# Optimization experiments

Hardware: AMD Instinct MI355X
Metric: run time of the kernel (lower is better)

Reference implementation:

```python
import jax, jax.numpy as jnp
import numpy as np

N_NODES = 10000
N_EDGES = 200000
STEPS = 2


def setup_inputs() -> dict:
    key = jax.random.key(0)
    ks = jax.random.split(key, 32)

    def w(k, shape):
        return jax.random.normal(k, shape, dtype=jnp.float32) * 0.05

    inp = {
        "x": jax.random.normal(ks[0], (N_NODES, 128), dtype=jnp.float32),
        "edge_attr": jax.random.normal(ks[1], (N_EDGES, 64), dtype=jnp.float32),
        "edge_index": jax.random.randint(ks[2], (2, N_EDGES), 0, N_NODES, dtype=jnp.int32),
        # node embedding MLP: 128 -> 128 -> 128 (ReLU after each, end_with_relu=True)
        "Wne1": w(ks[3], (128, 128)), "bne1": jnp.zeros((128,), jnp.float32),
        "Wne2": w(ks[4], (128, 128)), "bne2": jnp.zeros((128,), jnp.float32),
        # edge embedding MLP: 64 -> 128 -> 128
        "Wee1": w(ks[5], (64, 128)), "bee1": jnp.zeros((128,), jnp.float32),
        "Wee2": w(ks[6], (128, 128)), "bee2": jnp.zeros((128,), jnp.float32),
        # mlp_edge: (2*128*2 + 128*2)=768 -> 512 -> 128, ReLU after each
        "We1": w(ks[7], (768, 512)), "be1": jnp.zeros((512,), jnp.float32),
        "We2": w(ks[8], (512, 128)), "be2": jnp.zeros((128,), jnp.float32),
        # mlp_node: (128*2 + 128)=384 -> 128, ReLU
        "Wn1": w(ks[9], (384, 128)), "bn1": jnp.zeros((128,), jnp.float32),
        # update_mlp: 128 -> 128, ReLU
        "Wu": w(ks[10], (128, 128)), "bu": jnp.zeros((128,), jnp.float32),
        # node classification: 128 -> 128 (ReLU) -> 1
        "Wnc1": w(ks[11], (128, 128)), "bnc1": jnp.zeros((128,), jnp.float32),
        "Wnc2": w(ks[12], (128, 1)), "bnc2": jnp.zeros((1,), jnp.float32),
        # edge classification: 128 -> 128 (ReLU) -> 1
        "Wec1": w(ks[13], (128, 128)), "bec1": jnp.zeros((128,), jnp.float32),
        "Wec2": w(ks[14], (128, 1)), "bec2": jnp.zeros((1,), jnp.float32),
    }
    return inp


def reference(x, edge_attr, edge_index,
              Wne1, bne1, Wne2, bne2,
              Wee1, bee1, Wee2, bee2,
              We1, be1, We2, be2,
              Wn1, bn1, Wu, bu,
              Wnc1, bnc1, Wnc2, bnc2,
              Wec1, bec1, Wec2, bec2):
    relu = jax.nn.relu
    N = x.shape[0]
    j, i = edge_index[0], edge_index[1]  # j = source, i = target

    nf = relu(relu(x @ Wne1 + bne1) @ Wne2 + bne2)            # [N, 128]
    ef = relu(relu(edge_attr @ Wee1 + bee1) @ Wee2 + bee2)    # [E, 128]
    nf0, ef0 = nf, ef

    for _ in range(STEPS):
        # skip connections: concat initial features
        nfc = jnp.concatenate([nf0, nf], axis=1)   # [N, 256]
        efc = jnp.concatenate([ef0, ef], axis=1)   # [E, 256]
        x_i = nfc[i]                               # [E, 256] gather (target)
        x_j = nfc[j]                               # [E, 256] gather (source)
        # mlp_edge on [x_i, x_j, e_ij] -> new edge features [E, 128]
        e = relu(relu(jnp.concatenate([x_i, x_j, efc], axis=1) @ We1 + be1) @ We2 + be2)
        # message: mlp_node on [x_i, edge_attr] -> [E, 128]
        m = relu(jnp.concatenate([x_i, e], axis=1) @ Wn1 + bn1)
        # aggregate (add) messages at target nodes i
        agg = jax.ops.segment_sum(m, i, num_segments=N)       # [N, 128]
        # update MLP
        nf = relu(agg @ Wu + bu)
        ef = e

    preds_node = jnp.squeeze(relu(nf @ Wnc1 + bnc1) @ Wnc2 + bnc2)  # [N]
    preds_edge = jnp.squeeze(relu(ef @ Wec1 + bec1) @ Wec2 + bec2)  # [E]
    return (preds_edge, preds_node)
```

## Files before the change

kernel.cpp:

```cpp
#include <hip/hip_runtime.h>
#include <hip/hip_bf16.h>

#define N_NODES 10000
#define N_EDGES 200000
#define TE 32

typedef __attribute__((ext_vector_type(8))) short short8;
typedef __attribute__((ext_vector_type(4))) float f32x4;

static __device__ __forceinline__ ushort f2bf(float x) {
  union { float f; uint u; } v; v.f = x;
  uint r = v.u + 0x7FFF + ((v.u >> 16) & 1);
  return (ushort)(r >> 16);
}
static __device__ __forceinline__ float bf2f(ushort h) {
  union { uint u; float f; } v; v.u = ((uint)h) << 16;
  return v.f;
}

__global__ __launch_bounds__(256) void permute_w2(
    const float* __restrict__ W, ushort* __restrict__ Wp,
    int K, int N, int ld, int row0, int n0, int Ntot)
{
  int o = blockIdx.x * 256 + threadIdx.x;
  if (o >= K * N) return;
  int k = o & 31;
  int n = (o >> 5) % N;
  int kt = o / (N * 32);
  Wp[(size_t)kt * Ntot * 32 + (size_t)(n0 + n) * 32 + k] =
      f2bf(W[(size_t)(row0 + kt * 32 + k) * ld + n]);
}

template <int K1>
__global__ __launch_bounds__(256) void mlp2_kernel(
    const float* __restrict__ in, int n_rows,
    const float* __restrict__ W1, const float* __restrict__ b1,
    const float* __restrict__ W2, const float* __restrict__ b2,
    ushort* __restrict__ out0, ushort* __restrict__ out1)
{
  __shared__ float s_a[8][K1];
  __shared__ float s_h[8][128];
  const int r0 = blockIdx.x * 8;
  const int t = threadIdx.x;

  for (int idx = t; idx < 8 * K1; idx += 256) {
    int r = idx / K1, k = idx - r * K1;
    int row = r0 + r;
    s_a[r][k] = (row < n_rows) ? in[(size_t)row * K1 + k] : 0.f;
  }
  __syncthreads();

  const int c = t & 127;
  const int g = t >> 7;
  float acc[4];
#pragma unroll
  for (int e = 0; e < 4; ++e) acc[e] = b1[c];
  for (int k = 0; k < K1; ++k) {
    float w = W1[(size_t)k * 128 + c];
#pragma unroll
    for (int e = 0; e < 4; ++e) acc[e] = fmaf(s_a[g * 4 + e][k], w, acc[e]);
  }
#pragma unroll
  for (int e = 0; e < 4; ++e) s_h[g * 4 + e][c] = fmaxf(acc[e], 0.f);
  __syncthreads();

#pragma unroll
  for (int e = 0; e < 4; ++e) acc[e] = b2[c];
  for (int k = 0; k < 128; ++k) {
    float w = W2[(size_t)k * 128 + c];
#pragma unroll
    for (int e = 0; e < 4; ++e) acc[e] = fmaf(s_h[g * 4 + e][k], w, acc[e]);
  }
#pragma unroll
  for (int e = 0; e < 4; ++e) {
    int row = r0 + g * 4 + e;
    if (row < n_rows) {
      ushort v = f2bf(fmaxf(acc[e], 0.f));
      out0[(size_t)row * 128 + c] = v;
      if (out1) out1[(size_t)row * 128 + c] = v;
    }
  }
}

__global__ __launch_bounds__(256) void mlp1_kernel(
    const float* __restrict__ in, int n_rows,
    const float* __restrict__ W, const float* __restrict__ b,
    ushort* __restrict__ out)
{
  __shared__ float s_a[8][128];
  const int r0 = blockIdx.x * 8;
  const int t = threadIdx.x;
  for (int idx = t; idx < 8 * 128; idx += 256) {
    int r = idx >> 7, k = idx & 127;
    int row = r0 + r;
    s_a[r][k] = (row < n_rows) ? in[(size_t)row * 128 + k] : 0.f;
  }
  __syncthreads();
  const int c = t & 127;
  const int g = t >> 7;
  float acc[4];
#pragma unroll
  for (int e = 0; e < 4; ++e) acc[e] = b[c];
  for (int k = 0; k < 128; ++k) {
    float w = W[(size_t)k * 128 + c];
#pragma unroll
    for (int e = 0; e < 4; ++e) acc[e] = fmaf(s_a[g * 4 + e][k], w, acc[e]);
  }
#pragma unroll
  for (int e = 0; e < 4; ++e) {
    int row = r0 + g * 4 + e;
    if (row < n_rows) out[(size_t)row * 128 + c] = f2bf(fmaxf(acc[e], 0.f));
  }
}

__global__ __launch_bounds__(256) void cls_kernel(
    const ushort* __restrict__ feat, int n_rows,
    const float* __restrict__ W1, const float* __restrict__ b1,
    const float* __restrict__ W2, const float* __restrict__ b2,
    float* __restrict__ out)
{
  __shared__ float s_a[8][128];
  __shared__ float s_h[8][128];
  const int r0 = blockIdx.x * 8;
  const int t = threadIdx.x;
  for (int idx = t; idx < 8 * 128; idx += 256) {
    int r = idx >> 7, k = idx & 127;
    int row = r0 + r;
    s_a[r][k] = (row < n_rows) ? bf2f(feat[(size_t)row * 128 + k]) : 0.f;
  }
  __syncthreads();
  const int c = t & 127;
  const int g = t >> 7;
  float acc[4];
#pragma unroll
  for (int e = 0; e < 4; ++e) acc[e] = b1[c];
  for (int k = 0; k < 128; ++k) {
    float w = W1[(size_t)k * 128 + c];
#pragma unroll
    for (int e = 0; e < 4; ++e) acc[e] = fmaf(s_a[g * 4 + e][k], w, acc[e]);
  }
#pragma unroll
  for (int e = 0; e < 4; ++e) s_h[g * 4 + e][c] = fmaxf(acc[e], 0.f);
  __syncthreads();

  const int wave = t >> 6, lane = t & 63;
#pragma unroll
  for (int e2 = 0; e2 < 2; ++e2) {
    int r = wave * 2 + e2;
    float p = s_h[r][lane] * W2[lane] + s_h[r][lane + 64] * W2[lane + 64];
#pragma unroll
    for (int off = 32; off; off >>= 1) p += __shfl_down(p, off, 64);
    if (lane == 0) {
      int row = r0 + r;
      if (row < n_rows) out[row] = p + b2[0];
    }
  }
}

__global__ __launch_bounds__(256) void ee_mfma(
    const float* __restrict__ in,
    const ushort* __restrict__ W1p, const float* __restrict__ b1,
    const ushort* __restrict__ W2p, const float* __restrict__ b2,
    ushort* __restrict__ out0, ushort* __restrict__ out1)
{
  __shared__ char s_a[64 * 128];
  __shared__ char s_h[64 * 256];
  __shared__ ushort s_o[64 * 128];
  const int t = threadIdx.x;
  const int r0 = blockIdx.x * 64;

  for (int idx = t; idx < 512; idx += 256) {
    int r = idx >> 3, c8 = idx & 7;
    const float* src = in + (size_t)(r0 + r) * 64 + c8 * 8;
    float4 v0 = *(const float4*)src;
    float4 v1 = *(const float4*)(src + 4);
    ushort tmp[8] = {f2bf(v0.x), f2bf(v0.y), f2bf(v0.z), f2bf(v0.w),
                     f2bf(v1.x), f2bf(v1.y), f2bf(v1.z), f2bf(v1.w)};
    *(uint4*)(s_a + ((r * 128 + c8 * 16) ^ ((r & 7) << 4))) = *(uint4*)tmp;
  }
  __syncthreads();

  const int lane = t & 63, wave = t >> 6;
  const int r15 = lane & 15, g = lane >> 4;
  const int swz = (r15 & 7) << 4;
  const int arow = wave * 16 + r15;

  f32x4 h1[8];
#pragma unroll
  for (int j = 0; j < 8; ++j) { float bv = b1[j * 16 + r15]; h1[j] = (f32x4){bv, bv, bv, bv}; }
#pragma unroll
  for (int kt = 0; kt < 2; ++kt) {
    short8 a = *(const short8*)(s_a + ((arow * 128 + kt * 64 + g * 16) ^ swz));
    const ushort* wk = W1p + kt * 4096 + r15 * 32 + g * 8;
#pragma unroll
    for (int j = 0; j < 8; ++j) {
      short8 b = *(const short8*)(wk + j * 512);
      h1[j] = __builtin_amdgcn_mfma_f32_16x16x32_bf16(a, b, h1[j], 0, 0, 0);
    }
  }
#pragma unroll
  for (int j = 0; j < 8; ++j)
#pragma unroll
    for (int r = 0; r < 4; ++r) {
      int row = wave * 16 + g * 4 + r;
      int col = j * 16 + r15;
      *(ushort*)(s_h + ((row * 256 + col * 2) ^ ((row & 7) << 4))) = f2bf(fmaxf(h1[j][r], 0.f));
    }
  __syncthreads();

  f32x4 h2[8];
#pragma unroll
  for (int j = 0; j < 8; ++j) { float bv = b2[j * 16 + r15]; h2[j] = (f32x4){bv, bv, bv, bv}; }
#pragma unroll
  for (int kt = 0; kt < 4; ++kt) {
    short8 a = *(const short8*)(s_h + ((arow * 256 + kt * 64 + g * 16) ^ swz));
    const ushort* wk = W2p + kt * 4096 + r15 * 32 + g * 8;
#pragma unroll
    for (int j = 0; j < 8; ++j) {
      short8 b = *(const short8*)(wk + j * 512);
      h2[j] = __builtin_amdgcn_mfma_f32_16x16x32_bf16(a, b, h2[j], 0, 0, 0);
    }
  }
#pragma unroll
  for (int j = 0; j < 8; ++j)
#pragma unroll
    for (int r = 0; r < 4; ++r) {
      int row = wave * 16 + g * 4 + r;
      s_o[row * 128 + j * 16 + r15] = f2bf(fmaxf(h2[j][r], 0.f));
    }
  __syncthreads();
  for (int idx = t; idx < 1024; idx += 256) {
    int r = idx >> 4, c16 = idx & 15;
    uint4 v = *(uint4*)(&s_o[r * 128 + c16 * 8]);
    *(uint4*)(out0 + (size_t)(r0 + r) * 128 + c16 * 8) = v;
    *(uint4*)(out1 + (size_t)(r0 + r) * 128 + c16 * 8) = v;
  }
}

__global__ __launch_bounds__(256) void ec_mfma(
    const ushort* __restrict__ feat,
    const ushort* __restrict__ W1p, const float* __restrict__ b1,
    const float* __restrict__ W2, const float* __restrict__ b2,
    float* __restrict__ out)
{
  __shared__ char s_a[64 * 256];
  __shared__ float s_hf[64 * 132];
  const int t = threadIdx.x;
  const int r0 = blockIdx.x * 64;
  for (int idx = t; idx < 1024; idx += 256) {
    int r = idx >> 4, c16 = idx & 15;
    uint4 v = *(const uint4*)(feat + (size_t)(r0 + r) * 128 + c16 * 8);
    *(uint4*)(s_a + ((r * 256 + c16 * 16) ^ ((r & 7) << 4))) = v;
  }
  __syncthreads();
  const int lane = t & 63, wave = t >> 6;
  const int r15 = lane & 15, g = lane >> 4;
  const int swz = (r15 & 7) << 4;
  const int arow = wave * 16 + r15;

  f32x4 h1[8];
#pragma unroll
  for (int j = 0; j < 8; ++j) { float bv = b1[j * 16 + r15]; h1[j] = (f32x4){bv, bv, bv, bv}; }
#pragma unroll
  for (int kt = 0; kt < 4; ++kt) {
    short8 a = *(const short8*)(s_a + ((arow * 256 + kt * 64 + g * 16) ^ swz));
    const ushort* wk = W1p + kt * 4096 + r15 * 32 + g * 8;
#pragma unroll
    for (int j = 0; j < 8; ++j) {
      short8 b = *(const short8*)(wk + j * 512);
      h1[j] = __builtin_amdgcn_mfma_f32_16x16x32_bf16(a, b, h1[j], 0, 0, 0);
    }
  }
#pragma unroll
  for (int j = 0; j < 8; ++j)
#pragma unroll
    for (int r = 0; r < 4; ++r) {
      int row = wave * 16 + g * 4 + r;
      s_hf[row * 132 + j * 16 + r15] = fmaxf(h1[j][r], 0.f);
    }
  __syncthreads();
  {
    int row = t >> 2, q = t & 3;
    float p = 0.f;
#pragma unroll
    for (int c = 0; c < 32; ++c) {
      int col = q * 32 + c;
      p = fmaf(s_hf[row * 132 + col], W2[col], p);
    }
    p += __shfl_down(p, 1, 64);
    p += __shfl_down(p, 2, 64);
    if (q == 0) out[r0 + row] = p + b2[0];
  }
}

__global__ __launch_bounds__(256) void pre_mfma(
    const ushort* __restrict__ nf0, const ushort* __restrict__ nf,
    const ushort* __restrict__ Wsp, ushort* __restrict__ Ppack)
{
  __shared__ char s_a[64 * 512];
  const int t = threadIdx.x;
  const int r0 = blockIdx.x * 64;
  const int cc = blockIdx.y * 128;

  for (int idx = t; idx < 64 * 32; idx += 256) {
    int r = idx >> 5, c = idx & 31;
    int n = r0 + r; if (n >= N_NODES) n = N_NODES - 1;
    const ushort* base = (c < 16 ? nf0 : nf) + (size_t)n * 128 + (c & 15) * 8;
    *(uint4*)(s_a + ((r * 512 + c * 16) ^ ((r & 7) << 4))) = *(const uint4*)base;
  }
  __syncthreads();

  const int lane = t & 63, wave = t >> 6;
  const int r15 = lane & 15, g = lane >> 4;
  const int swz = (r15 & 7) << 4;

  f32x4 acc[8];
#pragma unroll
  for (int j = 0; j < 8; ++j) acc[j] = (f32x4){0.f, 0.f, 0.f, 0.f};
#pragma unroll
  for (int kt = 0; kt < 8; ++kt) {
    short8 a = *(const short8*)(s_a + (((wave * 16 + r15) * 512 + kt * 64 + g * 16) ^ swz));
    const ushort* wk = Wsp + (size_t)kt * 36864 + (size_t)(cc + r15) * 32 + g * 8;
#pragma unroll
    for (int j = 0; j < 8; ++j) {
      short8 b = *(const short8*)(wk + j * 512);
      acc[j] = __builtin_amdgcn_mfma_f32_16x16x32_bf16(a, b, acc[j], 0, 0, 0);
    }
  }
#pragma unroll
  for (int j = 0; j < 8; ++j)
#pragma unroll
    for (int r = 0; r < 4; ++r) {
      int row = r0 + wave * 16 + g * 4 + r;
      if (row < N_NODES)
        Ppack[(size_t)row * 1152 + cc + j * 16 + r15] = f2bf(acc[j][r]);
    }
}

__global__ __launch_bounds__(512, 4) void fused_edge_mfma(
    const ushort* __restrict__ Ppack,
    const ushort* __restrict__ ef0, ushort* __restrict__ ef,
    const int* __restrict__ ei,
    const ushort* __restrict__ W1ep, const float* __restrict__ be1,
    const ushort* __restrict__ W2p,  const float* __restrict__ be2,
    const ushort* __restrict__ W3ep, const float* __restrict__ bn1,
    float* __restrict__ agg)
{
  __shared__ __align__(16) char s_a[TE * 512];
  __shared__ __align__(16) char s_h[TE * 1024];
  __shared__ __align__(16) ushort s_q[TE * 136];
  __shared__ int s_i[TE], s_j[TE];

  const int t = threadIdx.x;
  const int NWG = N_EDGES / TE;
  const int q = NWG / 8, rr = NWG % 8;
  int xcd = blockIdx.x & 7, bidx = blockIdx.x >> 3;
  int wgid = (xcd < rr ? xcd * (q + 1) : rr * (q + 1) + (xcd - rr) * q) + bidx;
  const int e0 = wgid * TE;

  if (t < TE) s_j[t] = ei[e0 + t];
  else if (t < 2 * TE) s_i[t - TE] = ei[N_EDGES + e0 + (t - TE)];
  __syncthreads();

  for (int idx = t; idx < TE * 32; idx += 512) {
    int e = idx >> 5, c = idx & 31;
    const ushort* base = (c < 16 ? ef0 : ef) + (size_t)(e0 + e) * 128 + (c & 15) * 8;
    *(uint4*)(s_a + ((e * 512 + c * 16) ^ ((e & 7) << 4))) = *(const uint4*)base;
  }
  for (int idx = t; idx < TE * 64; idx += 512) {
    int e = idx >> 6, c = idx & 63;
    uint4 vi = *(const uint4*)(Ppack + (size_t)s_i[e] * 1152 + c * 8);
    uint4 vj = *(const uint4*)(Ppack + (size_t)s_j[e] * 1152 + 512 + c * 8);
    const ushort* pa = (const ushort*)&vi;
    const ushort* pb = (const ushort*)&vj;
    ushort o8[8];
#pragma unroll
    for (int z = 0; z < 8; ++z) o8[z] = f2bf(bf2f(pa[z]) + bf2f(pb[z]));
    *(uint4*)(s_h + ((e * 1024 + c * 16) ^ ((e & 7) << 4))) = *(uint4*)o8;
  }
  if (t < TE * 16) {
    int e = t >> 4, c = t & 15;
    uint4 v = *(const uint4*)(Ppack + (size_t)s_i[e] * 1152 + 1024 + c * 8);
    *(uint4*)((char*)s_q + e * 272 + c * 16) = v;
  }
  __syncthreads();

  const int lane = t & 63, wave = t >> 6;
  const int r15 = lane & 15, g = lane >> 4;
  const int swz = (r15 & 7) << 4;
  const int wb = wave * 64, wb2 = wave * 16;

  f32x4 acc1[2][4];
#pragma unroll
  for (int j = 0; j < 4; ++j) {
    float bv = be1[wb + j * 16 + r15];
#pragma unroll
    for (int mt = 0; mt < 2; ++mt)
#pragma unroll
      for (int r = 0; r < 4; ++r) {
        int row = mt * 16 + g * 4 + r;
        int col = wb + j * 16 + r15;
        ushort u = *(const ushort*)(s_h + ((row * 1024 + col * 2) ^ ((row & 7) << 4)));
        acc1[mt][j][r] = bv + bf2f(u);
      }
  }
  {
    const ushort* wkb = W1ep + (size_t)(wb + r15) * 32 + g * 8;
    short8 bc[4], bn[4];
#pragma unroll
    for (int j = 0; j < 4; ++j) bc[j] = *(const short8*)(wkb + j * 512);
    for (int kt = 0; kt < 8; ++kt) {
      short8 a0 = *(const short8*)(s_a + ((r15 * 512 + kt * 64 + g * 16) ^ swz));
      short8 a1 = *(const short8*)(s_a + (((r15 + 16) * 512 + kt * 64 + g * 16) ^ swz));
      const ushort* wnx = wkb + (size_t)(kt + 1) * 16384;
#pragma unroll
      for (int j = 0; j < 4; ++j) bn[j] = *(const short8*)(wnx + j * 512);
#pragma unroll
      for (int j = 0; j < 4; ++j) {
        acc1[0][j] = __builtin_amdgcn_mfma_f32_16x16x32_bf16(a0, bc[j], acc1[0][j], 0, 0, 0);
        acc1[1][j] = __builtin_amdgcn_mfma_f32_16x16x32_bf16(a1, bc[j], acc1[1][j], 0, 0, 0);
      }
#pragma unroll
      for (int j = 0; j < 4; ++j) bc[j] = bn[j];
    }
  }
#pragma unroll
  for (int mt = 0; mt < 2; ++mt)
#pragma unroll
    for (int j = 0; j < 4; ++j)
#pragma unroll
      for (int r = 0; r < 4; ++r) {
        int row = mt * 16 + g * 4 + r;
        int col = wb + j * 16 + r15;
        *(ushort*)(s_h + ((row * 1024 + col * 2) ^ ((row & 7) << 4))) =
            f2bf(fmaxf(acc1[mt][j][r], 0.f));
      }
  __syncthreads();

  f32x4 acc2[2], acc2b[2];
  {
    float bv = be2[wb2 + r15];
    acc2[0] = (f32x4){bv, bv, bv, bv};
    acc2[1] = (f32x4){bv, bv, bv, bv};
    acc2b[0] = (f32x4){0.f, 0.f, 0.f, 0.f};
    acc2b[1] = (f32x4){0.f, 0.f, 0.f, 0.f};
  }
  {
    const ushort* wkb = W2p + (size_t)(wb2 + r15) * 32 + g * 8;
    short8 bA = *(const short8*)(wkb);
    short8 bB = *(const short8*)(wkb + 4096);
    for (int kt2 = 0; kt2 < 8; ++kt2) {
      int ab0 = (2 * kt2) * 64 + g * 16;
      int ab1 = ab0 + 64;
      short8 a0e = *(const short8*)(s_h + ((r15 * 1024 + ab0) ^ swz));
      short8 a1e = *(const short8*)(s_h + (((r15 + 16) * 1024 + ab0) ^ swz));
      short8 a0o = *(const short8*)(s_h + ((r15 * 1024 + ab1) ^ swz));
      short8 a1o = *(const short8*)(s_h + (((r15 + 16) * 1024 + ab1) ^ swz));
      short8 bAn = *(const short8*)(wkb + (size_t)(2 * kt2 + 2) * 4096);
      short8 bBn = *(const short8*)(wkb + (size_t)(2 * kt2 + 3) * 4096);
      acc2[0]  = __builtin_amdgcn_mfma_f32_16x16x32_bf16(a0e, bA, acc2[0], 0, 0, 0);
      acc2b[0] = __builtin_amdgcn_mfma_f32_16x16x32_bf16(a0o, bB, acc2b[0], 0, 0, 0);
      acc2[1]  = __builtin_amdgcn_mfma_f32_16x16x32_bf16(a1e, bA, acc2[1], 0, 0, 0);
      acc2b[1] = __builtin_amdgcn_mfma_f32_16x16x32_bf16(a1o, bB, acc2b[1], 0, 0, 0);
      bA = bAn; bB = bBn;
    }
    acc2[0] = acc2[0] + acc2b[0];
    acc2[1] = acc2[1] + acc2b[1];
  }
#pragma unroll
  for (int mt = 0; mt < 2; ++mt)
#pragma unroll
    for (int r = 0; r < 4; ++r) {
      int row = mt * 16 + g * 4 + r;
      int col = wb2 + r15;
      *(ushort*)(s_a + ((row * 512 + col * 2) ^ ((row & 7) << 4))) =
          f2bf(fmaxf(acc2[mt][r], 0.f));
    }
  __syncthreads();

  if (t < TE * 16) {
    int e = t >> 4, c = t & 15;
    uint4 v = *(const uint4*)(s_a + ((e * 512 + c * 16) ^ ((e & 7) << 4)));
    *(uint4*)(ef + (size_t)(e0 + e) * 128 + c * 8) = v;
  }

  f32x4 acc3[2];
  {
    float bv = bn1[wb2 + r15];
#pragma unroll
    for (int mt = 0; mt < 2; ++mt)
#pragma unroll
      for (int r = 0; r < 4; ++r) {
        int row = mt * 16 + g * 4 + r;
        acc3[mt][r] = bv + bf2f(s_q[row * 136 + wb2 + r15]);
      }
  }
  {
    const ushort* w3b = W3ep + (size_t)(wb2 + r15) * 32 + g * 8;
    short8 bq[4];
#pragma unroll
    for (int kk = 0; kk < 4; ++kk) bq[kk] = *(const short8*)(w3b + (size_t)kk * 4096);
#pragma unroll
    for (int kk = 0; kk < 4; ++kk) {
      short8 a0 = *(const short8*)(s_a + ((r15 * 512 + kk * 64 + g * 16) ^ swz));
      short8 a1 = *(const short8*)(s_a + (((r15 + 16) * 512 + kk * 64 + g * 16) ^ swz));
      acc3[0] = __builtin_amdgcn_mfma_f32_16x16x32_bf16(a0, bq[kk], acc3[0], 0, 0, 0);
      acc3[1] = __builtin_amdgcn_mfma_f32_16x16x32_bf16(a1, bq[kk], acc3[1], 0, 0, 0);
    }
  }
#pragma unroll
  for (int mt = 0; mt < 2; ++mt)
#pragma unroll
    for (int r = 0; r < 4; ++r) {
      int row = mt * 16 + g * 4 + r;
      int node = s_i[row];
      atomicAdd(&agg[(size_t)node * 128 + wb2 + r15], fmaxf(acc3[mt][r], 0.f));
    }
}

extern "C" void kernel_launch(void* const* d_in, const int* in_sizes, int n_in,
                              void* d_out, int out_size, void* d_ws, size_t ws_size,
                              hipStream_t stream) {
  const float* x         = (const float*)d_in[0];
  const float* edge_attr = (const float*)d_in[1];
  const int*   ei        = (const int*)d_in[2];
  const float* Wne1 = (const float*)d_in[3];  const float* bne1 = (const float*)d_in[4];
  const float* Wne2 = (const float*)d_in[5];  const float* bne2 = (const float*)d_in[6];
  const float* Wee1 = (const float*)d_in[7];  const float* bee1 = (const float*)d_in[8];
  const float* Wee2 = (const float*)d_in[9];  const float* bee2 = (const float*)d_in[10];
  const float* We1  = (const float*)d_in[11]; const float* be1  = (const float*)d_in[12];
  const float* We2  = (const float*)d_in[13]; const float* be2  = (const float*)d_in[14];
  const float* Wn1  = (const float*)d_in[15]; const float* bn1  = (const float*)d_in[16];
  const float* Wu   = (const float*)d_in[17]; const float* bu   = (const float*)d_in[18];
  const float* Wnc1 = (const float*)d_in[19]; const float* bnc1 = (const float*)d_in[20];
  const float* Wnc2 = (const float*)d_in[21]; const float* bnc2 = (const float*)d_in[22];
  const float* Wec1 = (const float*)d_in[23]; const float* bec1 = (const float*)d_in[24];
  const float* Wec2 = (const float*)d_in[25]; const float* bec2 = (const float*)d_in[26];

  float* preds_edge = (float*)d_out;
  float* preds_node = preds_edge + N_EDGES;

  char* w = (char*)d_ws;
  ushort* nf0  = (ushort*)w; w += (size_t)N_NODES * 128 * 2;
  ushort* nf   = (ushort*)w; w += (size_t)N_NODES * 128 * 2;
  ushort* ef0  = (ushort*)w; w += (size_t)N_EDGES * 128 * 2;
  ushort* ef   = (ushort*)w; w += (size_t)N_EDGES * 128 * 2;
  float*  agg  = (float*)w;  w += (size_t)N_NODES * 128 * 4;
  ushort* Ppack = (ushort*)w; w += (size_t)N_NODES * 1152 * 2;
  ushort* Wsp  = (ushort*)w; w += (size_t)8 * 1152 * 32 * 2;
  ushort* W1ep = (ushort*)w; w += (size_t)9 * 512 * 32 * 2;
  ushort* W2p  = (ushort*)w; w += (size_t)18 * 128 * 32 * 2;
  ushort* W3ep = (ushort*)w; w += (size_t)4 * 128 * 32 * 2;
  ushort* Wee1p = (ushort*)w; w += (size_t)64 * 128 * 2;
  ushort* Wee2p = (ushort*)w; w += (size_t)128 * 128 * 2;
  ushort* Wec1p = (ushort*)w; w += (size_t)128 * 128 * 2;

  permute_w2<<<(256 * 512 + 255) / 256, 256, 0, stream>>>(We1, Wsp, 256, 512, 512, 0, 0, 1152);
  permute_w2<<<(256 * 512 + 255) / 256, 256, 0, stream>>>(We1, Wsp, 256, 512, 512, 256, 512, 1152);
  permute_w2<<<(256 * 128 + 255) / 256, 256, 0, stream>>>(Wn1, Wsp, 256, 128, 128, 0, 1024, 1152);
  permute_w2<<<(256 * 512 + 255) / 256, 256, 0, stream>>>(We1, W1ep, 256, 512, 512, 512, 0, 512);
  permute_w2<<<(512 * 128 + 255) / 256, 256, 0, stream>>>(We2, W2p, 512, 128, 128, 0, 0, 128);
  permute_w2<<<(128 * 128 + 255) / 256, 256, 0, stream>>>(Wn1, W3ep, 128, 128, 128, 256, 0, 128);
  permute_w2<<<(64 * 128 + 255) / 256, 256, 0, stream>>>(Wee1, Wee1p, 64, 128, 128, 0, 0, 128);
  permute_w2<<<(128 * 128 + 255) / 256, 256, 0, stream>>>(Wee2, Wee2p, 128, 128, 128, 0, 0, 128);
  permute_w2<<<(128 * 128 + 255) / 256, 256, 0, stream>>>(Wec1, Wec1p, 128, 128, 128, 0, 0, 128);

  mlp2_kernel<128><<<(N_NODES + 7) / 8, 256, 0, stream>>>(
      x, N_NODES, Wne1, bne1, Wne2, bne2, nf0, nf);
  ee_mfma<<<N_EDGES / 64, 256, 0, stream>>>(
      edge_attr, Wee1p, bee1, Wee2p, bee2, ef0, ef);

  for (int s = 0; s < 2; ++s) {
    pre_mfma<<<dim3((N_NODES + 63) / 64, 9), 256, 0, stream>>>(nf0, nf, Wsp, Ppack);
    hipMemsetAsync(agg, 0, (size_t)N_NODES * 128 * sizeof(float), stream);
    fused_edge_mfma<<<N_EDGES / TE, 512, 0, stream>>>(
        Ppack, ef0, ef, ei, W1ep, be1, W2p, be2, W3ep, bn1, agg);
    mlp1_kernel<<<(N_NODES + 7) / 8, 256, 0, stream>>>(agg, N_NODES, Wu, bu, nf);
  }

  ec_mfma<<<N_EDGES / 64, 256, 0, stream>>>(
      ef, Wec1p, bec1, Wec2, bec2, preds_edge);
  cls_kernel<<<(N_NODES + 7) / 8, 256, 0, stream>>>(
      nf, N_NODES, Wnc1, bnc1, Wnc2, bnc2, preds_node);
}
```

Baseline: 691.8 us.

## Overlap gathered node projections with first GEMM; merge weight permutes; drop ef copy

```diff
diff --git a/kernel.cpp b/kernel.cpp
--- a/kernel.cpp
+++ b/kernel.cpp
@@ -18,17 +18,37 @@
   return v.f;
 }
 
-__global__ __launch_bounds__(256) void permute_w2(
-    const float* __restrict__ W, ushort* __restrict__ Wp,
-    int K, int N, int ld, int row0, int n0, int Ntot)
-{
-  int o = blockIdx.x * 256 + threadIdx.x;
+__device__ __forceinline__ void permute_job(
+    const float* W, ushort* Wp, int o, int K, int N, int ld,
+    int row0, int n0, int Ntot)
+{
   if (o >= K * N) return;
   int k = o & 31;
   int n = (o >> 5) % N;
   int kt = o / (N * 32);
   Wp[(size_t)kt * Ntot * 32 + (size_t)(n0 + n) * 32 + k] =
       f2bf(W[(size_t)(row0 + kt * 32 + k) * ld + n]);
+}
+
+__global__ __launch_bounds__(256) void permute_all(
+    const float* __restrict__ We1, const float* __restrict__ We2,
+    const float* __restrict__ Wn1, const float* __restrict__ Wee1,
+    const float* __restrict__ Wee2, const float* __restrict__ Wec1,
+    ushort* __restrict__ Wsp, ushort* __restrict__ W1ep,
+    ushort* __restrict__ W2p, ushort* __restrict__ W3ep,
+    ushort* __restrict__ Wee1p, ushort* __restrict__ Wee2p,
+    ushort* __restrict__ Wec1p)
+{
+  int b = blockIdx.x, t = threadIdx.x;
+  if (b < 512)       permute_job(We1, Wsp,  (b       ) * 256 + t, 256, 512, 512,   0,    0, 1152);
+  else if (b < 1024) permute_job(We1, Wsp,  (b - 512 ) * 256 + t, 256, 512, 512, 256,  512, 1152);
+  else if (b < 1152) permute_job(Wn1, Wsp,  (b - 1024) * 256 + t, 256, 128, 128,   0, 1024, 1152);
+  else if (b < 1664) permute_job(We1, W1ep, (b - 1152) * 256 + t, 256, 512, 512, 512,    0,  512);
+  else if (b < 1920) permute_job(We2, W2p,  (b - 1664) * 256 + t, 512, 128, 128,   0,    0,  128);
+  else if (b < 1984) permute_job(Wn1, W3ep, (b - 1920) * 256 + t, 128, 128, 128, 256,    0,  128);
+  else if (b < 2016) permute_job(Wee1, Wee1p,(b - 1984) * 256 + t,  64, 128, 128,   0,    0,  128);
+  else if (b < 2080) permute_job(Wee2, Wee2p,(b - 2016) * 256 + t, 128, 128, 128,   0,    0,  128);
+  else               permute_job(Wec1, Wec1p,(b - 2080) * 256 + t, 128, 128, 128,   0,    0,  128);
 }
 
 template <int K1>
@@ -161,7 +181,7 @@
     const float* __restrict__ in,
     const ushort* __restrict__ W1p, const float* __restrict__ b1,
     const ushort* __restrict__ W2p, const float* __restrict__ b2,
-    ushort* __restrict__ out0, ushort* __restrict__ out1)
+    ushort* __restrict__ out0)
 {
   __shared__ char s_a[64 * 128];
   __shared__ char s_h[64 * 256];
@@ -233,7 +253,6 @@
     int r = idx >> 4, c16 = idx & 15;
     uint4 v = *(uint4*)(&s_o[r * 128 + c16 * 8]);
     *(uint4*)(out0 + (size_t)(r0 + r) * 128 + c16 * 8) = v;
-    *(uint4*)(out1 + (size_t)(r0 + r) * 128 + c16 * 8) = v;
   }
 }
 
@@ -339,7 +358,8 @@
 
 __global__ __launch_bounds__(512, 4) void fused_edge_mfma(
     const ushort* __restrict__ Ppack,
-    const ushort* __restrict__ ef0, ushort* __restrict__ ef,
+    const ushort* __restrict__ ef0, const ushort* __restrict__ efA,
+    ushort* __restrict__ ef,
     const int* __restrict__ ei,
     const ushort* __restrict__ W1ep, const float* __restrict__ be1,
     const ushort* __restrict__ W2p,  const float* __restrict__ be2,
@@ -362,26 +382,24 @@
   else if (t < 2 * TE) s_i[t - TE] = ei[N_EDGES + e0 + (t - TE)];
   __syncthreads();
 
+  uint4 vQ;
+  {
+    int e = t >> 4, c = t & 15;
+    vQ = *(const uint4*)(Ppack + (size_t)s_i[e] * 1152 + 1024 + c * 8);
+  }
+  uint4 vPi[4], vPj[4];
+#pragma unroll
+  for (int it = 0; it < 4; ++it) {
+    int idx = t + it * 512;
+    int e = idx >> 6, c = idx & 63;
+    vPi[it] = *(const uint4*)(Ppack + (size_t)s_i[e] * 1152 + c * 8);
+    vPj[it] = *(const uint4*)(Ppack + (size_t)s_j[e] * 1152 + 512 + c * 8);
+  }
+
   for (int idx = t; idx < TE * 32; idx += 512) {
     int e = idx >> 5, c = idx & 31;
-    const ushort* base = (c < 16 ? ef0 : ef) + (size_t)(e0 + e) * 128 + (c & 15) * 8;
+    const ushort* base = (c < 16 ? ef0 : efA) + (size_t)(e0 + e) * 128 + (c & 15) * 8;
     *(uint4*)(s_a + ((e * 512 + c * 16) ^ ((e & 7) << 4))) = *(const uint4*)base;
-  }
-  for (int idx = t; idx < TE * 64; idx += 512) {
-    int e = idx >> 6, c = idx & 63;
-    uint4 vi = *(const uint4*)(Ppack + (size_t)s_i[e] * 1152 + c * 8);
-    uint4 vj = *(const uint4*)(Ppack + (size_t)s_j[e] * 1152 + 512 + c * 8);
-    const ushort* pa = (const ushort*)&vi;
-    const ushort* pb = (const ushort*)&vj;
-    ushort o8[8];
-#pragma unroll
-    for (int z = 0; z < 8; ++z) o8[z] = f2bf(bf2f(pa[z]) + bf2f(pb[z]));
-    *(uint4*)(s_h + ((e * 1024 + c * 16) ^ ((e & 7) << 4))) = *(uint4*)o8;
-  }
-  if (t < TE * 16) {
-    int e = t >> 4, c = t & 15;
-    uint4 v = *(const uint4*)(Ppack + (size_t)s_i[e] * 1152 + 1024 + c * 8);
-    *(uint4*)((char*)s_q + e * 272 + c * 16) = v;
   }
   __syncthreads();
 
@@ -394,15 +412,8 @@
 #pragma unroll
   for (int j = 0; j < 4; ++j) {
     float bv = be1[wb + j * 16 + r15];
-#pragma unroll
-    for (int mt = 0; mt < 2; ++mt)
-#pragma unroll
-      for (int r = 0; r < 4; ++r) {
-        int row = mt * 16 + g * 4 + r;
-        int col = wb + j * 16 + r15;
-        ushort u = *(const ushort*)(s_h + ((row * 1024 + col * 2) ^ ((row & 7) << 4)));
-        acc1[mt][j][r] = bv + bf2f(u);
-      }
+    acc1[0][j] = (f32x4){bv, bv, bv, bv};
+    acc1[1][j] = (f32x4){bv, bv, bv, bv};
   }
   {
     const ushort* wkb = W1ep + (size_t)(wb + r15) * 32 + g * 8;
@@ -424,6 +435,24 @@
       for (int j = 0; j < 4; ++j) bc[j] = bn[j];
     }
   }
+
+#pragma unroll
+  for (int it = 0; it < 4; ++it) {
+    int idx = t + it * 512;
+    int e = idx >> 6, c = idx & 63;
+    const ushort* pa = (const ushort*)&vPi[it];
+    const ushort* pb = (const ushort*)&vPj[it];
+    ushort o8[8];
+#pragma unroll
+    for (int z = 0; z < 8; ++z) o8[z] = f2bf(bf2f(pa[z]) + bf2f(pb[z]));
+    *(uint4*)(s_h + ((e * 1024 + c * 16) ^ ((e & 7) << 4))) = *(uint4*)o8;
+  }
+  {
+    int e = t >> 4, c = t & 15;
+    *(uint4*)((char*)s_q + e * 272 + c * 16) = vQ;
+  }
+  __syncthreads();
+
 #pragma unroll
   for (int mt = 0; mt < 2; ++mt)
 #pragma unroll
@@ -432,8 +461,9 @@
       for (int r = 0; r < 4; ++r) {
         int row = mt * 16 + g * 4 + r;
         int col = wb + j * 16 + r15;
-        *(ushort*)(s_h + ((row * 1024 + col * 2) ^ ((row & 7) << 4))) =
-            f2bf(fmaxf(acc1[mt][j][r], 0.f));
+        char* p = s_h + ((row * 1024 + col * 2) ^ ((row & 7) << 4));
+        float v = acc1[mt][j][r] + bf2f(*(const ushort*)p);
+        *(ushort*)p = f2bf(fmaxf(v, 0.f));
       }
   __syncthreads();
 
@@ -478,7 +508,7 @@
     }
   __syncthreads();
 
-  if (t < TE * 16) {
+  {
     int e = t >> 4, c = t & 15;
     uint4 v = *(const uint4*)(s_a + ((e * 512 + c * 16) ^ ((e & 7) << 4)));
     *(uint4*)(ef + (size_t)(e0 + e) * 128 + c * 8) = v;
@@ -555,26 +585,21 @@
   ushort* Wee2p = (ushort*)w; w += (size_t)128 * 128 * 2;
   ushort* Wec1p = (ushort*)w; w += (size_t)128 * 128 * 2;
 
-  permute_w2<<<(256 * 512 + 255) / 256, 256, 0, stream>>>(We1, Wsp, 256, 512, 512, 0, 0, 1152);
-  permute_w2<<<(256 * 512 + 255) / 256, 256, 0, stream>>>(We1, Wsp, 256, 512, 512, 256, 512, 1152);
-  permute_w2<<<(256 * 128 + 255) / 256, 256, 0, stream>>>(Wn1, Wsp, 256, 128, 128, 0, 1024, 1152);
-  permute_w2<<<(256 * 512 + 255) / 256, 256, 0, stream>>>(We1, W1ep, 256, 512, 512, 512, 0, 512);
-  permute_w2<<<(512 * 128 + 255) / 256, 256, 0, stream>>>(We2, W2p, 512, 128, 128, 0, 0, 128);
-  permute_w2<<<(128 * 128 + 255) / 256, 256, 0, stream>>>(Wn1, W3ep, 128, 128, 128, 256, 0, 128);
-  permute_w2<<<(64 * 128 + 255) / 256, 256, 0, stream>>>(Wee1, Wee1p, 64, 128, 128, 0, 0, 128);
-  permute_w2<<<(128 * 128 + 255) / 256, 256, 0, stream>>>(Wee2, Wee2p, 128, 128, 128, 0, 0, 128);
-  permute_w2<<<(128 * 128 + 255) / 256, 256, 0, stream>>>(Wec1, Wec1p, 128, 128, 128, 0, 0, 128);
+  permute_all<<<2144, 256, 0, stream>>>(
+      We1, We2, Wn1, Wee1, Wee2, Wec1,
+      Wsp, W1ep, W2p, W3ep, Wee1p, Wee2p, Wec1p);
 
   mlp2_kernel<128><<<(N_NODES + 7) / 8, 256, 0, stream>>>(
       x, N_NODES, Wne1, bne1, Wne2, bne2, nf0, nf);
   ee_mfma<<<N_EDGES / 64, 256, 0, stream>>>(
-      edge_attr, Wee1p, bee1, Wee2p, bee2, ef0, ef);
+      edge_attr, Wee1p, bee1, Wee2p, bee2, ef0);
 
   for (int s = 0; s < 2; ++s) {
     pre_mfma<<<dim3((N_NODES + 63) / 64, 9), 256, 0, stream>>>(nf0, nf, Wsp, Ppack);
     hipMemsetAsync(agg, 0, (size_t)N_NODES * 128 * sizeof(float), stream);
     fused_edge_mfma<<<N_EDGES / TE, 512, 0, stream>>>(
-        Ppack, ef0, ef, ei, W1ep, be1, W2p, be2, W3ep, bn1, agg);
+        Ppack, ef0, (s == 0 ? ef0 : ef), ef, ei,
+        W1ep, be1, W2p, be2, W3ep, bn1, agg);
     mlp1_kernel<<<(N_NODES + 7) / 8, 256, 0, stream>>>(agg, N_NODES, Wu, bu, nf);
   }
 
```

Measured after the change: 706.0 us. 1.02x slower.
